# Performance work log

Measured on AMD Instinct MI355X. Metric: run time of the kernel, lower is better.

## Reference

```python
import jax, jax.numpy as jnp
import numpy as np
from jax import lax

EPS = 1e-5


def _bn_eval(x, gamma, beta, mean, var, axis=1):
    # eval-mode batchnorm over channel axis
    shape = [1] * x.ndim
    shape[axis] = -1
    g = gamma.reshape(shape); b = beta.reshape(shape)
    m = mean.reshape(shape); v = var.reshape(shape)
    return (x - m) * (g * lax.rsqrt(v + EPS)) + b


def setup_inputs() -> dict:
    key = jax.random.key(0)
    ks = jax.random.split(key, 12)
    B, C, H, W, K = 16, 256, 128, 128, 5
    x_feat = jax.random.normal(ks[0], (B, C, H, W), jnp.float32)
    raw_img = jax.random.uniform(ks[1], (B, 3, H, W), jnp.float32)
    # img_feature: Conv2d(3,64,3,pad=1) + BN(64)
    w_conv1 = jax.random.normal(ks[2], (64, 3, 3, 3), jnp.float32) * 0.1
    b_conv1 = jax.random.normal(ks[3], (64,), jnp.float32) * 0.1
    g1 = jnp.ones((64,), jnp.float32)
    beta1 = jnp.zeros((64,), jnp.float32)
    m1 = jax.random.normal(ks[4], (64,), jnp.float32) * 0.1
    v1 = jax.random.uniform(ks[5], (64,), jnp.float32) + 0.5
    # conv_filter: Conv2d(64, C*K*K, 1) + BN(C*K*K)
    CK2 = C * K * K
    w_filt = jax.random.normal(ks[6], (CK2, 64), jnp.float32) * 0.05
    b_filt = jax.random.normal(ks[7], (CK2,), jnp.float32) * 0.05
    g2 = jnp.ones((CK2,), jnp.float32)
    beta2 = jnp.zeros((CK2,), jnp.float32)
    m2 = jax.random.normal(ks[8], (CK2,), jnp.float32) * 0.1
    v2 = jax.random.uniform(ks[9], (CK2,), jnp.float32) + 0.5
    return {"x_feat": x_feat, "raw_img": raw_img,
            "w_conv1": w_conv1, "b_conv1": b_conv1, "g1": g1, "beta1": beta1, "m1": m1, "v1": v1,
            "w_filt": w_filt, "b_filt": b_filt, "g2": g2, "beta2": beta2, "m2": m2, "v2": v2}


def reference(x_feat, raw_img, w_conv1, b_conv1, g1, beta1, m1, v1,
              w_filt, b_filt, g2, beta2, m2, v2):
    B, C, H, W = x_feat.shape
    K = int(round(np.sqrt(w_filt.shape[0] // C)))  # kernel_size
    pad = K // 2

    # ---- filter generation branch ----
    # Conv2d(3,64,3,pad=1)
    y = lax.conv_general_dilated(raw_img, w_conv1, (1, 1), ((1, 1), (1, 1)),
                                 dimension_numbers=("NCHW", "OIHW", "NCHW"))
    y = y + b_conv1[None, :, None, None]
    y = jax.nn.relu(_bn_eval(y, g1, beta1, m1, v1))
    img_feat = jnp.mean(y, axis=(2, 3))                        # (B, 64) global avg pool

    # 1x1 conv == dense: (B, C*K*K)
    df = img_feat @ w_filt.T + b_filt
    df = _bn_eval(df[:, :, None, None], g2, beta2, m2, v2)[:, :, 0, 0]
    df = df.reshape(B, C, K * K)
    # NOTE: original applies Softmax(dim=1) -> over the CHANNEL axis
    df = jax.nn.softmax(df, axis=1)                            # (B, C, K*K)

    # ---- per-sample dynamic depthwise conv ----
    x_pad = jnp.pad(x_feat, ((0, 0), (0, 0), (pad, pad), (pad, pad)), mode="reflect")
    filt = df.reshape(B, C, K, K)

    def dw(x, w):  # x: (C, Hp, Wp), w: (C, K, K)
        return lax.conv_general_dilated(
            x[None], w[:, None], (1, 1), "VALID",
            dimension_numbers=("NCHW", "OIHW", "NCHW"),
            feature_group_count=C)[0]

    out = jax.vmap(dw)(x_pad, filt)                            # (B, C, H, W)
    return out
```

## Files before the change

### kernel.cpp

```cpp
#include <hip/hip_runtime.h>

#define EPSV 1e-5f

typedef float f4 __attribute__((ext_vector_type(4)));
typedef float f2 __attribute__((ext_vector_type(2)));

#define B   16
#define CIN 3
#define C1  64
#define C   256
#define H   128
#define W   128
#define K   5
#define KK  25
#define FSTR 28

__global__ __launch_bounds__(256) void k0_prep(
    const float* __restrict__ wconv, const float* __restrict__ bconv,
    const float* __restrict__ g1, const float* __restrict__ be1,
    const float* __restrict__ m1, const float* __restrict__ v1,
    const float* __restrict__ wf,
    float* __restrict__ wconvT, float* __restrict__ Ag,
    float* __restrict__ Bg, float* __restrict__ wfT)
{
  const int bid = blockIdx.x, tid = threadIdx.x;
  if (bid < 100) {
    const int kk = bid >> 2;
    const int c0 = (bid & 3) << 6;
    __shared__ float tl[64][65];
    for (int i = tid; i < 64 * 64; i += 256) {
      int cl = i >> 6, j = i & 63;
      tl[cl][j] = wf[((size_t)(c0 + cl) * KK + kk) * C1 + j];
    }
    __syncthreads();
    for (int i = tid; i < 64 * 64; i += 256) {
      int j = i >> 6, cl = i & 63;
      wfT[(size_t)j * (C * KK) + kk * C + c0 + cl] = tl[cl][j];
    }
  } else {
    for (int i = tid; i < 27 * 64; i += 256) {
      int k = i >> 6, c = i & 63;
      wconvT[k * 64 + c] = wconv[c * 27 + k];
    }
    if (tid < C1) {
      float sc = g1[tid] * rsqrtf(v1[tid] + EPSV);
      Ag[tid] = sc;
      Bg[tid] = (bconv[tid] - m1[tid]) * sc + be1[tid];
    }
  }
}

#define R1   8
#define WS1  32
#define TW1  36

__global__ __launch_bounds__(128) void k1_conv_pool(
    const float* __restrict__ raw, const float* __restrict__ wconvT,
    const float* __restrict__ Ag, const float* __restrict__ Bg,
    float* __restrict__ partial)
{
  const int bid   = blockIdx.x;
  const int b     = bid >> 6;
  const int chunk = (bid >> 2) & 15;
  const int wh    = bid & 3;
  const int tid   = threadIdx.x;

  __shared__ __align__(16) float t[CIN][R1 + 2][TW1];
  const float* rawb = raw + (size_t)b * CIN * H * W;
  for (int i = tid; i < CIN * (R1 + 2) * 34; i += 128) {
    int ic  = i / ((R1 + 2) * 34);
    int rem = i - ic * (R1 + 2) * 34;
    int r   = rem / 34;
    int cc  = rem - r * 34;
    int gr  = chunk * R1 + r - 1;
    int gc  = wh * WS1 + cc - 1;
    float val = 0.f;
    if ((unsigned)gr < H && (unsigned)gc < W)
      val = rawb[ic * H * W + gr * W + gc];
    t[ic][r][cc] = val;
  }
  __syncthreads();

  const int rp  = tid >> 5;
  const int grp = tid & 31;
  float wt[2][27], A[2], Bc[2];
#pragma unroll
  for (int k = 0; k < 27; ++k) {
    wt[0][k] = wconvT[k * 64 + grp * 2];
    wt[1][k] = wconvT[k * 64 + grp * 2 + 1];
  }
#pragma unroll
  for (int g = 0; g < 2; ++g) {
    A[g]  = Ag[grp * 2 + g];
    Bc[g] = Bg[grp * 2 + g];
  }

  f4 cur[CIN][4], nxt[CIN][4];
#pragma unroll
  for (int ic = 0; ic < CIN; ++ic)
#pragma unroll
    for (int r = 0; r < 4; ++r) cur[ic][r] = *(const f4*)&t[ic][2 * rp + r][0];

  float acc0 = 0.f, acc1 = 0.f;
#pragma unroll
  for (int j = 0; j < 8; ++j) {
#pragma unroll
    for (int ic = 0; ic < CIN; ++ic)
#pragma unroll
      for (int r = 0; r < 4; ++r) nxt[ic][r] = *(const f4*)&t[ic][2 * rp + r][4 * j + 4];

    float v[2][2][4];
#pragma unroll
    for (int q = 0; q < 2; ++q)
#pragma unroll
      for (int g = 0; g < 2; ++g)
#pragma unroll
        for (int p = 0; p < 4; ++p) v[q][g][p] = 0.f;

#pragma unroll
    for (int ic = 0; ic < CIN; ++ic) {
#pragma unroll
      for (int q = 0; q < 2; ++q) {
#pragma unroll
        for (int kh = 0; kh < 3; ++kh) {
          f4 a  = cur[ic][q + kh];
          f4 bb = nxt[ic][q + kh];
#pragma unroll
          for (int p = 0; p < 4; ++p) {
#pragma unroll
            for (int kw = 0; kw < 3; ++kw) {
              float e = (p + kw < 4) ? a[p + kw] : bb[p + kw - 4];
              v[q][0][p] += e * wt[0][ic * 9 + kh * 3 + kw];
              v[q][1][p] += e * wt[1][ic * 9 + kh * 3 + kw];
            }
          }
        }
      }
    }
#pragma unroll
    for (int q = 0; q < 2; ++q)
#pragma unroll
      for (int p = 0; p < 4; ++p) {
        acc0 += fmaxf(v[q][0][p] * A[0] + Bc[0], 0.f);
        acc1 += fmaxf(v[q][1][p] * A[1] + Bc[1], 0.f);
      }
#pragma unroll
    for (int ic = 0; ic < CIN; ++ic)
#pragma unroll
      for (int r = 0; r < 4; ++r) cur[ic][r] = nxt[ic][r];
  }

  __shared__ float red[4][C1];
  red[rp][grp * 2]     = acc0;
  red[rp][grp * 2 + 1] = acc1;
  __syncthreads();
  if (tid < C1) {
    float s = red[0][tid] + red[1][tid] + red[2][tid] + red[3][tid];
    partial[((size_t)((b * 16 + chunk) * 4 + wh)) * C1 + tid] = s;
  }
}

#define NCH 64

__global__ __launch_bounds__(256) void k2_filter(
    const float* __restrict__ partial, const float* __restrict__ wfT,
    const float* __restrict__ bf, const float* __restrict__ g2,
    const float* __restrict__ be2, const float* __restrict__ m2,
    const float* __restrict__ v2, float* __restrict__ filt)
{
  const int b  = blockIdx.x / KK;
  const int kk = blockIdx.x - b * KK;
  const int c  = threadIdx.x;

  __shared__ float feat[C1];
  if (c < C1) {
    float s = 0.f;
#pragma unroll
    for (int ch = 0; ch < NCH; ++ch)
      s += partial[((size_t)b * NCH + ch) * C1 + c];
    feat[c] = s * (1.f / (H * W));
  }
  __syncthreads();

  const int idx = c * KK + kk;
  float v = bf[idx];
#pragma unroll
  for (int j = 0; j < C1; ++j)
    v += feat[j] * wfT[(size_t)j * (C * KK) + kk * C + c];
  v = (v - m2[idx]) * (g2[idx] * rsqrtf(v2[idx] + EPSV)) + be2[idx];

  __shared__ float red[256];
  red[c] = v;
  __syncthreads();
#pragma unroll
  for (int s = 128; s > 0; s >>= 1) {
    if (c < s) red[c] = fmaxf(red[c], red[c + s]);
    __syncthreads();
  }
  float mx = red[0];
  __syncthreads();
  float e = expf(v - mx);
  red[c] = e;
  __syncthreads();
#pragma unroll
  for (int s = 128; s > 0; s >>= 1) {
    if (c < s) red[c] += red[c + s];
    __syncthreads();
  }
  filt[((size_t)b * C + c) * FSTR + kk] = e / red[0];
}

#define R3  32
#define TH3 36

__global__ __launch_bounds__(256, 6) void k3_dwconv(
    const float* __restrict__ x, const float* __restrict__ filt,
    float* __restrict__ out)
{
  const int bid = blockIdx.x;
  const int swz = (bid & 7) * 2048 + (bid >> 3);
  const int plane = swz >> 2;
  const int tile  = swz & 3;
  const int r0    = tile * R3;
  const int tid   = threadIdx.x;
  const int lane  = tid & 63;
  const int wv    = tid >> 6;

  const float* xp = x   + (size_t)plane * H * W;
  float*       op = out + (size_t)plane * H * W;
  const float* fp = filt + (size_t)plane * FSTR;

  f4 fv[7];
#pragma unroll
  for (int i = 0; i < 7; ++i) fv[i] = *(const f4*)&fp[i << 2];

  __shared__ __align__(16) float t[TH3][W];

  for (int i = wv; i < TH3 / 2; i += 4) {
    int r  = 2 * i + (lane >> 5);
    int gr = r0 + r - 2;
    gr = gr < 0 ? -gr : (gr >= H ? 2 * H - 2 - gr : gr);
    const float* gsrc = xp + gr * W + ((lane & 31) << 2);
    __builtin_amdgcn_global_load_lds(
        (const __attribute__((address_space(1))) void*)gsrc,
        (__attribute__((address_space(3))) void*)&t[2 * i][0],
        16, 0, 0);
  }
  __syncthreads();

  const int g    = tid & 31;
  const int w    = g << 2;
  const bool edge = (g == 31);
  const int bcol = edge ? 0   : w + 4;
  const int colA = edge ? 126 : w + 2;
  const int colB = edge ? 0   : w + 4;
  const int rb   = (tid >> 5) << 2;

  f4 acc[4];
#pragma unroll
  for (int q = 0; q < 4; ++q) acc[q] = (f4){0.f, 0.f, 0.f, 0.f};

#pragma unroll
  for (int tr = 0; tr < 8; ++tr) {
    f4 a  = *(const f4*)&t[rb + tr][w];
    f4 bb = *(const f4*)&t[rb + tr][bcol];
    float wa[6], wb[6];
    wa[0] = a[0]; wa[1] = a[1]; wa[2] = a[2]; wa[3] = a[3];
    wa[4] = edge ? a[2]  : bb[0];
    wa[5] = edge ? a[1]  : bb[1];
    wb[0] = edge ? bb[2] : a[2];
    wb[1] = edge ? bb[1] : a[3];
    wb[2] = bb[0]; wb[3] = bb[1]; wb[4] = bb[2]; wb[5] = bb[3];
#pragma unroll
    for (int q = 0; q < 4; ++q) {
      if (tr - q < 0 || tr - q > 4) continue;
      const int ki = tr - q;
#pragma unroll
      for (int j = 0; j < 5; ++j) {
        const int kq = ki * 5 + j;
        const float fk = fv[kq >> 2][kq & 3];
        acc[q][0] += wa[j]     * fk;
        acc[q][1] += wa[j + 1] * fk;
        acc[q][2] += wb[j]     * fk;
        acc[q][3] += wb[j + 1] * fk;
      }
    }
  }
#pragma unroll
  for (int q = 0; q < 4; ++q) {
    const int row = r0 + rb + q;
    f2 vA = {acc[q][0], acc[q][1]};
    f2 vB = {acc[q][2], acc[q][3]};
    __builtin_nontemporal_store(vA, (f2*)&op[row * W + colA]);
    __builtin_nontemporal_store(vB, (f2*)&op[row * W + colB]);
  }
}

extern "C" void kernel_launch(void* const* d_in, const int* in_sizes, int n_in,
                              void* d_out, int out_size, void* d_ws, size_t ws_size,
                              hipStream_t stream) {
  const float* x_feat = (const float*)d_in[0];
  const float* raw    = (const float*)d_in[1];
  const float* wconv  = (const float*)d_in[2];
  const float* bconv  = (const float*)d_in[3];
  const float* g1     = (const float*)d_in[4];
  const float* be1    = (const float*)d_in[5];
  const float* m1     = (const float*)d_in[6];
  const float* v1     = (const float*)d_in[7];
  const float* wf     = (const float*)d_in[8];
  const float* bf     = (const float*)d_in[9];
  const float* g2     = (const float*)d_in[10];
  const float* be2    = (const float*)d_in[11];
  const float* m2     = (const float*)d_in[12];
  const float* v2     = (const float*)d_in[13];
  float* out = (float*)d_out;

  float* partial = (float*)d_ws;
  float* filt    = partial + B * NCH * C1;
  float* wconvT  = filt + B * C * FSTR;
  float* Ag      = wconvT + 27 * 64;
  float* Bg      = Ag + 64;
  float* wfT     = Bg + 64;

  k0_prep    <<<101, 256, 0, stream>>>(wconv, bconv, g1, be1, m1, v1, wf,
                                       wconvT, Ag, Bg, wfT);
  k1_conv_pool<<<B * 16 * 4, 128, 0, stream>>>(raw, wconvT, Ag, Bg, partial);
  k2_filter  <<<B * KK, 256, 0, stream>>>(partial, wfT, bf, g2, be2, m2, v2, filt);
  k3_dwconv  <<<B * C * (H / R3), 256, 0, stream>>>(x_feat, filt, out);
}
```

Measured before the change: 124.3 us.

## Process whole plane per block with double-buffered LDS staging of row tiles

The depthwise conv kernel now assigns one full 128x128 plane to each block instead of one 32-row tile, looping over four tiles. A double-buffered shared-memory array lets the async global-to-LDS copy of the next tile overlap with computation on the current one. The filter is loaded once per plane, and the grid shrinks fourfold. In exchange, LDS per block doubles, occupancy hint drops to 4 blocks, and there are fewer blocks to balance across CUs.

```diff
diff --git a/kernel.cpp b/kernel.cpp
--- a/kernel.cpp
+++ b/kernel.cpp
@@ -213,15 +213,61 @@
 #define R3  32
 #define TH3 36
 
-__global__ __launch_bounds__(256, 6) void k3_dwconv(
+#define STAGE(bufi, r0s)                                                      \
+  for (int i = wv; i < TH3 / 2; i += 4) {                                     \
+    int r  = 2 * i + (lane >> 5);                                             \
+    int gr = (r0s) + r - 2;                                                   \
+    gr = gr < 0 ? -gr : (gr >= H ? 2 * H - 2 - gr : gr);                      \
+    const float* gsrc = xp + gr * W + ((lane & 31) << 2);                     \
+    __builtin_amdgcn_global_load_lds(                                         \
+        (const __attribute__((address_space(1))) void*)gsrc,                  \
+        (__attribute__((address_space(3))) void*)&t[bufi][2 * i][0],          \
+        16, 0, 0);                                                            \
+  }
+
+#define COMPUTE(bufi, r0s)                                                    \
+  {                                                                           \
+    f4 acc[4];                                                                \
+    _Pragma("unroll") for (int q = 0; q < 4; ++q)                             \
+      acc[q] = (f4){0.f, 0.f, 0.f, 0.f};                                      \
+    _Pragma("unroll") for (int tr = 0; tr < 8; ++tr) {                        \
+      f4 a  = *(const f4*)&t[bufi][rb + tr][w];                               \
+      f4 bb = *(const f4*)&t[bufi][rb + tr][bcol];                            \
+      float wa[6], wb[6];                                                     \
+      wa[0] = a[0]; wa[1] = a[1]; wa[2] = a[2]; wa[3] = a[3];                 \
+      wa[4] = edge ? a[2]  : bb[0];                                           \
+      wa[5] = edge ? a[1]  : bb[1];                                           \
+      wb[0] = edge ? bb[2] : a[2];                                            \
+      wb[1] = edge ? bb[1] : a[3];                                            \
+      wb[2] = bb[0]; wb[3] = bb[1]; wb[4] = bb[2]; wb[5] = bb[3];             \
+      _Pragma("unroll") for (int q = 0; q < 4; ++q) {                         \
+        if (tr - q < 0 || tr - q > 4) continue;                               \
+        const int ki = tr - q;                                                \
+        _Pragma("unroll") for (int j = 0; j < 5; ++j) {                       \
+          const int kq = ki * 5 + j;                                          \
+          const float fk = fv[kq >> 2][kq & 3];                               \
+          acc[q][0] += wa[j]     * fk;                                        \
+          acc[q][1] += wa[j + 1] * fk;                                        \
+          acc[q][2] += wb[j]     * fk;                                        \
+          acc[q][3] += wb[j + 1] * fk;                                        \
+        }                                                                     \
+      }                                                                       \
+    }                                                                         \
+    _Pragma("unroll") for (int q = 0; q < 4; ++q) {                           \
+      const int row = (r0s) + rb + q;                                         \
+      f2 vA = {acc[q][0], acc[q][1]};                                         \
+      f2 vB = {acc[q][2], acc[q][3]};                                         \
+      __builtin_nontemporal_store(vA, (f2*)&op[row * W + colA]);              \
+      __builtin_nontemporal_store(vB, (f2*)&op[row * W + colB]);              \
+    }                                                                         \
+  }
+
+__global__ __launch_bounds__(256, 4) void k3_dwconv(
     const float* __restrict__ x, const float* __restrict__ filt,
     float* __restrict__ out)
 {
-  const int bid = blockIdx.x;
-  const int swz = (bid & 7) * 2048 + (bid >> 3);
-  const int plane = swz >> 2;
-  const int tile  = swz & 3;
-  const int r0    = tile * R3;
+  const int bid   = blockIdx.x;
+  const int plane = (bid & 7) * 512 + (bid >> 3);
   const int tid   = threadIdx.x;
   const int lane  = tid & 63;
   const int wv    = tid >> 6;
@@ -234,19 +280,7 @@
 #pragma unroll
   for (int i = 0; i < 7; ++i) fv[i] = *(const f4*)&fp[i << 2];
 
-  __shared__ __align__(16) float t[TH3][W];
-
-  for (int i = wv; i < TH3 / 2; i += 4) {
-    int r  = 2 * i + (lane >> 5);
-    int gr = r0 + r - 2;
-    gr = gr < 0 ? -gr : (gr >= H ? 2 * H - 2 - gr : gr);
-    const float* gsrc = xp + gr * W + ((lane & 31) << 2);
-    __builtin_amdgcn_global_load_lds(
-        (const __attribute__((address_space(1))) void*)gsrc,
-        (__attribute__((address_space(3))) void*)&t[2 * i][0],
-        16, 0, 0);
-  }
-  __syncthreads();
+  __shared__ __align__(16) float t[2][TH3][W];
 
   const int g    = tid & 31;
   const int w    = g << 2;
@@ -256,44 +290,22 @@
   const int colB = edge ? 0   : w + 4;
   const int rb   = (tid >> 5) << 2;
 
-  f4 acc[4];
-#pragma unroll
-  for (int q = 0; q < 4; ++q) acc[q] = (f4){0.f, 0.f, 0.f, 0.f};
-
-#pragma unroll
-  for (int tr = 0; tr < 8; ++tr) {
-    f4 a  = *(const f4*)&t[rb + tr][w];
-    f4 bb = *(const f4*)&t[rb + tr][bcol];
-    float wa[6], wb[6];
-    wa[0] = a[0]; wa[1] = a[1]; wa[2] = a[2]; wa[3] = a[3];
-    wa[4] = edge ? a[2]  : bb[0];
-    wa[5] = edge ? a[1]  : bb[1];
-    wb[0] = edge ? bb[2] : a[2];
-    wb[1] = edge ? bb[1] : a[3];
-    wb[2] = bb[0]; wb[3] = bb[1]; wb[4] = bb[2]; wb[5] = bb[3];
-#pragma unroll
-    for (int q = 0; q < 4; ++q) {
-      if (tr - q < 0 || tr - q > 4) continue;
-      const int ki = tr - q;
-#pragma unroll
-      for (int j = 0; j < 5; ++j) {
-        const int kq = ki * 5 + j;
-        const float fk = fv[kq >> 2][kq & 3];
-        acc[q][0] += wa[j]     * fk;
-        acc[q][1] += wa[j + 1] * fk;
-        acc[q][2] += wb[j]     * fk;
-        acc[q][3] += wb[j + 1] * fk;
-      }
-    }
-  }
-#pragma unroll
-  for (int q = 0; q < 4; ++q) {
-    const int row = r0 + rb + q;
-    f2 vA = {acc[q][0], acc[q][1]};
-    f2 vB = {acc[q][2], acc[q][3]};
-    __builtin_nontemporal_store(vA, (f2*)&op[row * W + colA]);
-    __builtin_nontemporal_store(vB, (f2*)&op[row * W + colB]);
-  }
+  STAGE(0, 0)
+  __syncthreads();
+
+  STAGE(1, 32)
+  COMPUTE(0, 0)
+  __syncthreads();
+
+  STAGE(0, 64)
+  COMPUTE(1, 32)
+  __syncthreads();
+
+  STAGE(1, 96)
+  COMPUTE(0, 64)
+  __syncthreads();
+
+  COMPUTE(1, 96)
 }
 
 extern "C" void kernel_launch(void* const* d_in, const int* in_sizes, int n_in,
@@ -326,5 +338,5 @@
                                        wconvT, Ag, Bg, wfT);
   k1_conv_pool<<<B * 16 * 4, 128, 0, stream>>>(raw, wconvT, Ag, Bg, partial);
   k2_filter  <<<B * KK, 256, 0, stream>>>(partial, wfT, bf, g2, be2, m2, v2, filt);
-  k3_dwconv  <<<B * C * (H / R3), 256, 0, stream>>>(x_feat, filt, out);
-}
+  k3_dwconv  <<<B * C, 256, 0, stream>>>(x_feat, filt, out);
+}
```

New measurement: 125.6 us. About the same (+1.1%).
